# Kernel tuning notes

Hardware: AMD Instinct MI355X
Metric: run time of the kernel (lower is better)

Reference implementation:

```python
import jax, jax.numpy as jnp
import numpy as np

T, B, IN, H, BODY = 512, 256, 128, 512, 64
ALPHA = 10.0 / 100.0  # dt / tau


def setup_inputs() -> dict:
    key = jax.random.key(0)
    ks = jax.random.split(key, 9)
    s = 0.05
    return {
        "x": jax.random.normal(ks[0], (T, B, IN), dtype=jnp.float32),
        "W_i2h": jax.random.normal(ks[1], (H, IN), dtype=jnp.float32) * s,
        "b_i2h": jax.random.normal(ks[2], (H,), dtype=jnp.float32) * s,
        "W_h2h": jax.random.normal(ks[3], (H, H), dtype=jnp.float32) * s,
        "b_h2h": jax.random.normal(ks[4], (H,), dtype=jnp.float32) * s,
        "W_b2h": jax.random.normal(ks[5], (H, BODY), dtype=jnp.float32) * s,
        "b_b2h": jax.random.normal(ks[6], (H,), dtype=jnp.float32) * s,
        "W_h2b": jax.random.normal(ks[7], (BODY, H), dtype=jnp.float32) * s,
        "b_h2b": jax.random.normal(ks[8], (BODY,), dtype=jnp.float32) * s,
        "body_mask": jnp.ones((BODY,), dtype=jnp.float32),
    }


def reference(x, W_i2h, b_i2h, W_h2h, b_h2h, W_b2h, b_b2h, W_h2b, b_h2b, body_mask):
    # Precompute input projection for all timesteps (one big GEMM).
    x_proj = jnp.einsum("tbi,hi->tbh", x, W_i2h) + b_i2h  # [T,B,H]

    def step(carry, xp_t):
        h, b = carry
        pre = xp_t + h @ W_h2h.T + b_h2h + b @ W_b2h.T + b_b2h
        h_new = jax.nn.relu(pre)
        h_new = h * (1.0 - ALPHA) + h_new * ALPHA
        b_new = b * body_mask + ALPHA * (h @ W_h2b.T + b_h2b)
        return (h_new, b_new), (h_new, b_new)

    h0 = jnp.zeros((B, H), dtype=x.dtype)
    b0 = jnp.zeros((B, BODY), dtype=x.dtype)
    (h_fin, _), (hidden_out, body_out) = jax.lax.scan(step, (h0, b0), x_proj)
    return hidden_out, body_out, h_fin
```

## Files before the change

### kernel.cpp

```cpp
#include <hip/hip_runtime.h>


#define T_STEPS 512
#define NB      256
#define IN_DIM  128
#define HID     512
#define BODYD   64
#define ALPHA_F 0.1f

#define WS_WH    0u
#define WS_WH2   524288u
#define WS_WI    1048576u
#define WS_WHB   1179648u
#define WS_WHB2  1245184u
#define WS_WBH   1310720u
#define WS_WBH2  1376256u
#define WS_BIAS  1441792u
#define WS_FLAG  1443840u
#define WS_XCHG  1476608u
#define GRP_STRIDE 73728u

#define BODY_OFF 67108864u
#define FIN_OFF  75497472u

typedef __attribute__((ext_vector_type(8))) short bf16x8;
typedef __attribute__((ext_vector_type(4))) float f32x4;

__device__ __forceinline__ unsigned short f2bf(float f) {
    union { float f; unsigned int u; } v; v.f = f;
    unsigned int u = v.u;
    return (unsigned short)((u + 0x7fffu + ((u >> 16) & 1u)) >> 16);
}
__device__ __forceinline__ float b2f(unsigned short h) {
    union { unsigned int u; float f; } v; v.u = ((unsigned int)h) << 16;
    return v.f;
}
__device__ __forceinline__ bf16x8 ldfrag(const unsigned short* p) {
    return *reinterpret_cast<const bf16x8*>(p);
}

#define LD128_SYSP(dst, ptr)                                           \
    asm volatile("global_load_dwordx4 %0, %1, off sc0 sc1"             \
                 : "=v"(dst) : "v"(ptr) : "memory")
#define ST16_SYS(base, imm, val)                                           \
    asm volatile("global_store_short %0, %1, off offset:" #imm " sc0 sc1"  \
                 :: "v"(base), "v"((unsigned int)(val)) : "memory")

__global__ void init_kernel(const float* __restrict__ Wi2h, const float* __restrict__ bi2h,
                            const float* __restrict__ Whh,  const float* __restrict__ bh2h,
                            const float* __restrict__ Wb2h, const float* __restrict__ bb2h,
                            const float* __restrict__ Wh2b,
                            unsigned char* __restrict__ ws) {
    int idx = blockIdx.x * blockDim.x + threadIdx.x;
    int stride = gridDim.x * blockDim.x;
    unsigned short* WH  = (unsigned short*)(ws + WS_WH);
    unsigned short* WH2 = (unsigned short*)(ws + WS_WH2);
    for (int i = idx; i < HID * HID; i += stride) {
        float w = Whh[i]; unsigned short h = f2bf(w);
        WH[i] = h; WH2[i] = f2bf(w - b2f(h));
    }
    unsigned short* WI = (unsigned short*)(ws + WS_WI);
    for (int i = idx; i < HID * IN_DIM; i += stride) WI[i] = f2bf(Wi2h[i]);
    unsigned short* WHB  = (unsigned short*)(ws + WS_WHB);
    unsigned short* WHB2 = (unsigned short*)(ws + WS_WHB2);
    for (int i = idx; i < BODYD * HID; i += stride) {
        float w = Wh2b[i]; unsigned short h = f2bf(w);
        WHB[i] = h; WHB2[i] = f2bf(w - b2f(h));
    }
    unsigned short* WBH  = (unsigned short*)(ws + WS_WBH);
    unsigned short* WBH2 = (unsigned short*)(ws + WS_WBH2);
    for (int i = idx; i < HID * BODYD; i += stride) {
        float w = Wb2h[i]; unsigned short h = f2bf(w);
        WBH[i] = h; WBH2[i] = f2bf(w - b2f(h));
    }
    float* BS = (float*)(ws + WS_BIAS);
    for (int i = idx; i < HID; i += stride) BS[i] = bi2h[i] + bh2h[i] + bb2h[i];
    unsigned int* Z = (unsigned int*)(ws + WS_FLAG);
    int zn = (int)((WS_XCHG + 32u * GRP_STRIDE - WS_FLAG) / 4u);
    for (int i = idx; i < zn; i += stride) Z[i] = 0u;
}

__global__ __launch_bounds__(256) void xproj_kernel(const float* __restrict__ x,
                                                    float* __restrict__ out,
                                                    const unsigned char* __restrict__ ws) {
    const unsigned short* WI = (const unsigned short*)(ws + WS_WI);
    const float* BS = (const float*)(ws + WS_BIAS);
    int tid = threadIdx.x;
    int l = tid & 63, ww = tid >> 6;
    int lr = l & 15, lq = l >> 4;
    int m0 = blockIdx.x * 64 + ww * 16;
    int n0 = blockIdx.y * 128;

    bf16x8 a[4];
    const float* xr = x + (size_t)(m0 + lr) * IN_DIM + lq * 8;
#pragma unroll
    for (int kt = 0; kt < 4; ++kt) {
        bf16x8 t;
#pragma unroll
        for (int e = 0; e < 8; ++e) t[e] = (short)f2bf(xr[kt * 32 + e]);
        a[kt] = t;
    }
    f32x4 acc[8];
#pragma unroll
    for (int jt = 0; jt < 8; ++jt) acc[jt] = (f32x4){0.f, 0.f, 0.f, 0.f};
#pragma unroll
    for (int jt = 0; jt < 8; ++jt) {
        const unsigned short* wr = WI + (size_t)(n0 + jt * 16 + lr) * IN_DIM + lq * 8;
#pragma unroll
        for (int kt = 0; kt < 4; ++kt) {
            bf16x8 b = ldfrag(wr + kt * 32);
            acc[jt] = __builtin_amdgcn_mfma_f32_16x16x32_bf16(a[kt], b, acc[jt], 0, 0, 0);
        }
    }
#pragma unroll
    for (int jt = 0; jt < 8; ++jt) {
        int n = n0 + jt * 16 + lr;
        float bs = BS[n];
#pragma unroll
        for (int i = 0; i < 4; ++i) {
            int mm = m0 + lq * 4 + i;
            out[(size_t)mm * HID + n] = acc[jt][i] + bs;
        }
    }
}

__global__ __launch_bounds__(512, 2) void rnn_kernel(float* __restrict__ out,
                                                     unsigned char* __restrict__ ws,
                                                     const float* __restrict__ bh2b,
                                                     const float* __restrict__ mask) {
    const int tid = threadIdx.x;
    const int l = tid & 63;
    const int ww = tid >> 6;
    const int jt = ww >> 1;
    const int kh = ww & 1;
    const int lr = l & 15;
    const int lq = l >> 4;

    const int w = blockIdx.x;
    const int xcd = w & 7;
    const int slot = w >> 3;
    const int g = (slot >> 3) * 8 + xcd;
    const int m = slot & 7;

    __shared__ f32x4 stg[1152];
    __shared__ f32x4 lds_h[4][64];
    __shared__ f32x4 lds_b[8][64];
    unsigned char* stgb = (unsigned char*)stg;

    const unsigned short* WH  = (const unsigned short*)(ws + WS_WH);
    const unsigned short* WH2 = (const unsigned short*)(ws + WS_WH2);
    bf16x8 wh[8], wh2[8];
    const int wrow = m * 64 + jt * 16 + lr;
    {
        const unsigned short* p1 = WH  + (size_t)wrow * HID + kh * 256 + lq * 8;
        const unsigned short* p2 = WH2 + (size_t)wrow * HID + kh * 256 + lq * 8;
#pragma unroll
        for (int r = 0; r < 8; ++r) { wh[r] = ldfrag(p1 + r * 32); wh2[r] = ldfrag(p2 + r * 32); }
    }
    const unsigned short* WBH  = (const unsigned short*)(ws + WS_WBH);
    const unsigned short* WBH2 = (const unsigned short*)(ws + WS_WBH2);
    bf16x8 wbh  = ldfrag(WBH  + (size_t)wrow * BODYD + kh * 32 + lq * 8);
    bf16x8 wbh2 = ldfrag(WBH2 + (size_t)wrow * BODYD + kh * 32 + lq * 8);

    bf16x8 whb0 = {}, whb1 = {}, whb0l = {}, whb1l = {};
    float maskv = 0.f, bhbv = 0.f;
    const int kt0 = kh * 8 + 2 * jt;
    if (m < 4) {
        const unsigned short* WHB  = (const unsigned short*)(ws + WS_WHB);
        const unsigned short* WHB2 = (const unsigned short*)(ws + WS_WHB2);
        const int brow = m * 16 + lr;
        whb0  = ldfrag(WHB  + (size_t)brow * HID + kt0 * 32 + lq * 8);
        whb1  = ldfrag(WHB  + (size_t)brow * HID + (kt0 + 1) * 32 + lq * 8);
        whb0l = ldfrag(WHB2 + (size_t)brow * HID + kt0 * 32 + lq * 8);
        whb1l = ldfrag(WHB2 + (size_t)brow * HID + (kt0 + 1) * 32 + lq * 8);
        maskv = mask[m * 16 + lr];
        bhbv  = bh2b[m * 16 + lr];
    }

    unsigned char* xg = ws + WS_XCHG + (size_t)g * GRP_STRIDE;
    unsigned int* flg_self = (unsigned int*)(ws + WS_FLAG) + g * 256 + m * 32;
    unsigned int* flg_base = (unsigned int*)(ws + WS_FLAG) + g * 256;
    unsigned int* flg_mine = flg_base + ww * 32;

    float hst[4] = {0.f, 0.f, 0.f, 0.f};
    float bst[4] = {0.f, 0.f, 0.f, 0.f};

    const int jg = m * 64 + jt * 16 + lr;

    const int c8 = l >> 3;
    const int r8 = l & 7;
    const unsigned char* ghb = xg + (size_t)r8 * 1024 + ww * 128 + c8 * 16;
    unsigned char* sth = stgb + (ww * 8 + c8) * 128 + r8 * 16;
    const int cc = (l >> 3) & 1;
    const unsigned char* gbb = xg + 65536u + (size_t)r8 * 128 + ww * 32 + cc * 16;
    unsigned char* stb = stgb + 16384 + (ww * 2 + cc) * 128 + r8 * 16;
    const bool bl = (ww < 4) && (l < 16);

    const unsigned char* fhb = stgb + kh * 4096 + lq * 128 + (lr & 7) * 16;
    const unsigned char* fbb = stgb + 16384 + (kh * 4 + lq) * 128 + (lr & 7) * 16;

    for (int t = 0; t < T_STEPS; ++t) {
        const int p = t & 1;

        if (t > 0) {
            while (__hip_atomic_load(flg_mine, __ATOMIC_RELAXED,
                                     __HIP_MEMORY_SCOPE_SYSTEM) < (unsigned int)t) {
                __builtin_amdgcn_s_sleep(1);
            }
        }

        const unsigned char* ghp = ghb + (size_t)p * 32768u;
        f32x4 vh1, vh2, vb1, vb2;
        LD128_SYSP(vh1, ghp);
        LD128_SYSP(vh2, ghp + 16384);
        if (bl) {
            const unsigned char* gbp = gbb + (size_t)p * 4096u;
            LD128_SYSP(vb1, gbp);
            LD128_SYSP(vb2, gbp + 2048);
        }
        asm volatile("s_waitcnt vmcnt(0)" ::: "memory");
        __builtin_amdgcn_sched_barrier(0);
        *(f32x4*)sth = vh1;
        *(f32x4*)(sth + 8192) = vh2;
        if (bl) { *(f32x4*)stb = vb1; *(f32x4*)(stb + 1024) = vb2; }
        __syncthreads();

        bf16x8 a[8], a2[8], ab1, ab2;
#pragma unroll
        for (int r = 0; r < 8; ++r) {
            a[r]  = *(const bf16x8*)(fhb + r * 512);
            a2[r] = *(const bf16x8*)(fhb + 8192 + r * 512);
        }
        ab1 = *(const bf16x8*)fbb;
        ab2 = *(const bf16x8*)(fbb + 1024);

        float cpre[4] = {0.f, 0.f, 0.f, 0.f};
        float* op = out + (size_t)t * (NB * HID) + (size_t)(g * 8) * HID + jg;
        if (!kh && lq < 2) {
#pragma unroll
            for (int i = 0; i < 4; ++i)
                cpre[i] = __builtin_nontemporal_load(op + (size_t)(lq * 4 + i) * HID);
        }

        f32x4 acc0 = {0.f, 0.f, 0.f, 0.f}, acc1 = acc0, acc2 = acc0;
#pragma unroll
        for (int r = 0; r < 8; ++r) acc0 = __builtin_amdgcn_mfma_f32_16x16x32_bf16(a[r],  wh[r],  acc0, 0, 0, 0);
#pragma unroll
        for (int r = 0; r < 8; ++r) acc1 = __builtin_amdgcn_mfma_f32_16x16x32_bf16(a2[r], wh[r],  acc1, 0, 0, 0);
#pragma unroll
        for (int r = 0; r < 8; ++r) acc2 = __builtin_amdgcn_mfma_f32_16x16x32_bf16(a[r],  wh2[r], acc2, 0, 0, 0);
        acc0 = __builtin_amdgcn_mfma_f32_16x16x32_bf16(ab1, wbh,  acc0, 0, 0, 0);
        acc1 = __builtin_amdgcn_mfma_f32_16x16x32_bf16(ab2, wbh,  acc1, 0, 0, 0);
        acc2 = __builtin_amdgcn_mfma_f32_16x16x32_bf16(ab1, wbh2, acc2, 0, 0, 0);
        f32x4 acc = acc0 + acc1 + acc2;

        f32x4 bacc = {0.f, 0.f, 0.f, 0.f};
        if (m < 4) {
            bf16x8 s0, s1, u0, u1;
            if      (jt == 0) { s0 = a[0]; s1 = a[1]; u0 = a2[0]; u1 = a2[1]; }
            else if (jt == 1) { s0 = a[2]; s1 = a[3]; u0 = a2[2]; u1 = a2[3]; }
            else if (jt == 2) { s0 = a[4]; s1 = a[5]; u0 = a2[4]; u1 = a2[5]; }
            else              { s0 = a[6]; s1 = a[7]; u0 = a2[6]; u1 = a2[7]; }
            f32x4 b0 = {0.f, 0.f, 0.f, 0.f}, b1 = b0;
            b0 = __builtin_amdgcn_mfma_f32_16x16x32_bf16(s0, whb0,  b0, 0, 0, 0);
            b1 = __builtin_amdgcn_mfma_f32_16x16x32_bf16(s1, whb1,  b1, 0, 0, 0);
            b0 = __builtin_amdgcn_mfma_f32_16x16x32_bf16(u0, whb0,  b0, 0, 0, 0);
            b1 = __builtin_amdgcn_mfma_f32_16x16x32_bf16(u1, whb1,  b1, 0, 0, 0);
            b0 = __builtin_amdgcn_mfma_f32_16x16x32_bf16(s0, whb0l, b0, 0, 0, 0);
            b1 = __builtin_amdgcn_mfma_f32_16x16x32_bf16(s1, whb1l, b1, 0, 0, 0);
            bacc = b0 + b1;
        }

        if (kh) lds_h[jt][l] = acc;
        if (m < 4) lds_b[ww][l] = bacc;
        __syncthreads();

        float hnv[4] = {0.f, 0.f, 0.f, 0.f};
        float bnv[4] = {0.f, 0.f, 0.f, 0.f};

        if (!kh) {
            f32x4 oth = lds_h[jt][l];
            f32x4 sum = acc + oth;
            if (lq < 2) {
                unsigned short* q1 = (unsigned short*)(xg + ((p ^ 1) * 2 + 0) * 16384)
                                     + (lq * 4) * HID + jg;
                unsigned short* q2 = (unsigned short*)(xg + ((p ^ 1) * 2 + 1) * 16384)
                                     + (lq * 4) * HID + jg;
                unsigned short hh[4], hl[4];
#pragma unroll
                for (int i = 0; i < 4; ++i) {
                    float pre = sum[i] + cpre[i];
                    float rl = fmaxf(pre, 0.f);
                    float hv = 0.9f * hst[i] + 0.1f * rl;
                    hst[i] = hv; hnv[i] = hv;
                    hh[i] = f2bf(hv); hl[i] = f2bf(hv - b2f(hh[i]));
                }
                ST16_SYS(q1, 0,    hh[0]); ST16_SYS(q1, 1024, hh[1]);
                ST16_SYS(q1, 2048, hh[2]); ST16_SYS(q1, 3072, hh[3]);
                ST16_SYS(q2, 0,    hl[0]); ST16_SYS(q2, 1024, hl[1]);
                ST16_SYS(q2, 2048, hl[2]); ST16_SYS(q2, 3072, hl[3]);
            }
        }
        if (ww == 0 && m < 4) {
            f32x4 bs = lds_b[0][l];
#pragma unroll
            for (int s = 1; s < 8; ++s) bs += lds_b[s][l];
            if (lq < 2) {
                int jb = m * 16 + lr;
                unsigned short* r1 = (unsigned short*)(xg + 65536 + ((p ^ 1) * 2 + 0) * 2048)
                                     + (lq * 4) * BODYD + jb;
                unsigned short* r2 = (unsigned short*)(xg + 65536 + ((p ^ 1) * 2 + 1) * 2048)
                                     + (lq * 4) * BODYD + jb;
                unsigned short bh[4], blo[4];
#pragma unroll
                for (int i = 0; i < 4; ++i) {
                    float bn = bst[i] * maskv + ALPHA_F * (bs[i] + bhbv);
                    bst[i] = bn; bnv[i] = bn;
                    bh[i] = f2bf(bn); blo[i] = f2bf(bn - b2f(bh[i]));
                }
                ST16_SYS(r1, 0,   bh[0]);  ST16_SYS(r1, 128, bh[1]);
                ST16_SYS(r1, 256, bh[2]);  ST16_SYS(r1, 384, bh[3]);
                ST16_SYS(r2, 0,   blo[0]); ST16_SYS(r2, 128, blo[1]);
                ST16_SYS(r2, 256, blo[2]); ST16_SYS(r2, 384, blo[3]);
            }
        }

        asm volatile("s_waitcnt vmcnt(0)" ::: "memory");
        __syncthreads();

        if (tid == 0) {
            __hip_atomic_store(flg_self, (unsigned int)(t + 1),
                               __ATOMIC_RELAXED, __HIP_MEMORY_SCOPE_SYSTEM);
        }

        if (!kh && lq < 2) {
#pragma unroll
            for (int i = 0; i < 4; ++i)
                __builtin_nontemporal_store(hnv[i], op + (size_t)(lq * 4 + i) * HID);
        }
        if (ww == 0 && m < 4 && lq < 2) {
            int jb = m * 16 + lr;
#pragma unroll
            for (int i = 0; i < 4; ++i) {
                int mi = lq * 4 + i;
                __builtin_nontemporal_store(
                    bnv[i],
                    out + BODY_OFF + (size_t)t * (NB * BODYD) + (size_t)(g * 8 + mi) * BODYD + jb);
            }
        }
    }

    if (!kh && lq < 2) {
#pragma unroll
        for (int i = 0; i < 4; ++i) {
            int mi = lq * 4 + i;
            __builtin_nontemporal_store(hst[i], out + FIN_OFF + (size_t)(g * 8 + mi) * HID + jg);
        }
    }
}

extern "C" void kernel_launch(void* const* d_in, const int* in_sizes, int n_in,
                              void* d_out, int out_size, void* d_ws, size_t ws_size,
                              hipStream_t stream) {
    const float* x    = (const float*)d_in[0];
    const float* Wi2h = (const float*)d_in[1];
    const float* bi2h = (const float*)d_in[2];
    const float* Whh  = (const float*)d_in[3];
    const float* bh2h = (const float*)d_in[4];
    const float* Wb2h = (const float*)d_in[5];
    const float* bb2h = (const float*)d_in[6];
    const float* Wh2b = (const float*)d_in[7];
    const float* bh2b = (const float*)d_in[8];
    const float* mask = (const float*)d_in[9];
    float* out = (float*)d_out;
    unsigned char* ws = (unsigned char*)d_ws;

    init_kernel<<<256, 256, 0, stream>>>(Wi2h, bi2h, Whh, bh2h, Wb2h, bb2h, Wh2b, ws);
    xproj_kernel<<<dim3(2048, 4), 256, 0, stream>>>(x, out, ws);

    void* kargs[] = { (void*)&out, (void*)&ws, (void*)&bh2b, (void*)&mask };
    hipLaunchCooperativeKernel((void*)rnn_kernel, dim3(256), dim3(512), kargs, 0, stream);
}
```

Baseline: 1.777 ms.

## Replace per-block flag with per-wave flags to drop end-of-step block barrier

Each wave that produces hidden or body state now publishes its own completion flag right after its stores drain, instead of waiting on a block-wide __syncthreads and a single flag from thread 0. Consumers poll several per-wave flags in parallel lanes (lanes 0-4) rather than one block flag. Body reduction moves from wave 0 to wave 1 to spread work. This removes a block barrier from the per-timestep critical path, at the cost of more flag traffic and more polling loads per step.

```diff
diff --git a/kernel.cpp b/kernel.cpp
--- a/kernel.cpp
+++ b/kernel.cpp
@@ -180,7 +180,6 @@
     unsigned char* xg = ws + WS_XCHG + (size_t)g * GRP_STRIDE;
     unsigned int* flg_self = (unsigned int*)(ws + WS_FLAG) + g * 256 + m * 32;
     unsigned int* flg_base = (unsigned int*)(ws + WS_FLAG) + g * 256;
-    unsigned int* flg_mine = flg_base + ww * 32;
 
     float hst[4] = {0.f, 0.f, 0.f, 0.f};
     float bst[4] = {0.f, 0.f, 0.f, 0.f};
@@ -191,9 +190,8 @@
     const int r8 = l & 7;
     const unsigned char* ghb = xg + (size_t)r8 * 1024 + ww * 128 + c8 * 16;
     unsigned char* sth = stgb + (ww * 8 + c8) * 128 + r8 * 16;
-    const int cc = (l >> 3) & 1;
-    const unsigned char* gbb = xg + 65536u + (size_t)r8 * 128 + ww * 32 + cc * 16;
-    unsigned char* stb = stgb + 16384 + (ww * 2 + cc) * 128 + r8 * 16;
+    const unsigned char* gbb = xg + 65536u + (size_t)r8 * 128 + ww * 32 + ((l >> 3) & 1) * 16;
+    unsigned char* stb = stgb + 16384 + (ww * 2 + ((l >> 3) & 1)) * 128 + r8 * 16;
     const bool bl = (ww < 4) && (l < 16);
 
     const unsigned char* fhb = stgb + kh * 4096 + lq * 128 + (lr & 7) * 16;
@@ -203,9 +201,13 @@
         const int p = t & 1;
 
         if (t > 0) {
-            while (__hip_atomic_load(flg_mine, __ATOMIC_RELAXED,
-                                     __HIP_MEMORY_SCOPE_SYSTEM) < (unsigned int)t) {
-                __builtin_amdgcn_s_sleep(1);
+            const bool need = (l < 4) || ((l == 4) && (ww < 4));
+            if (need) {
+                unsigned int* f = flg_base + ww * 32 + l;
+                while (__hip_atomic_load(f, __ATOMIC_RELAXED,
+                                         __HIP_MEMORY_SCOPE_SYSTEM) < (unsigned int)t) {
+                    __builtin_amdgcn_s_sleep(1);
+                }
             }
         }
 
@@ -275,12 +277,10 @@
         if (m < 4) lds_b[ww][l] = bacc;
         __syncthreads();
 
-        float hnv[4] = {0.f, 0.f, 0.f, 0.f};
-        float bnv[4] = {0.f, 0.f, 0.f, 0.f};
-
         if (!kh) {
             f32x4 oth = lds_h[jt][l];
             f32x4 sum = acc + oth;
+            float hnv[4] = {0.f, 0.f, 0.f, 0.f};
             if (lq < 2) {
                 unsigned short* q1 = (unsigned short*)(xg + ((p ^ 1) * 2 + 0) * 16384)
                                      + (lq * 4) * HID + jg;
@@ -300,13 +300,25 @@
                 ST16_SYS(q2, 0,    hl[0]); ST16_SYS(q2, 1024, hl[1]);
                 ST16_SYS(q2, 2048, hl[2]); ST16_SYS(q2, 3072, hl[3]);
             }
-        }
-        if (ww == 0 && m < 4) {
+            asm volatile("s_waitcnt vmcnt(0)" ::: "memory");
+            if (l == 0) {
+                __hip_atomic_store(flg_self + jt, (unsigned int)(t + 1),
+                                   __ATOMIC_RELAXED, __HIP_MEMORY_SCOPE_SYSTEM);
+            }
+            if (lq < 2) {
+#pragma unroll
+                for (int i = 0; i < 4; ++i)
+                    __builtin_nontemporal_store(hnv[i], op + (size_t)(lq * 4 + i) * HID);
+            }
+        }
+
+        if (ww == 1 && m < 4) {
             f32x4 bs = lds_b[0][l];
 #pragma unroll
             for (int s = 1; s < 8; ++s) bs += lds_b[s][l];
+            float bnv[4] = {0.f, 0.f, 0.f, 0.f};
+            int jb = m * 16 + lr;
             if (lq < 2) {
-                int jb = m * 16 + lr;
                 unsigned short* r1 = (unsigned short*)(xg + 65536 + ((p ^ 1) * 2 + 0) * 2048)
                                      + (lq * 4) * BODYD + jb;
                 unsigned short* r2 = (unsigned short*)(xg + 65536 + ((p ^ 1) * 2 + 1) * 2048)
@@ -323,29 +335,20 @@
                 ST16_SYS(r2, 0,   blo[0]); ST16_SYS(r2, 128, blo[1]);
                 ST16_SYS(r2, 256, blo[2]); ST16_SYS(r2, 384, blo[3]);
             }
-        }
-
-        asm volatile("s_waitcnt vmcnt(0)" ::: "memory");
-        __syncthreads();
-
-        if (tid == 0) {
-            __hip_atomic_store(flg_self, (unsigned int)(t + 1),
-                               __ATOMIC_RELAXED, __HIP_MEMORY_SCOPE_SYSTEM);
-        }
-
-        if (!kh && lq < 2) {
-#pragma unroll
-            for (int i = 0; i < 4; ++i)
-                __builtin_nontemporal_store(hnv[i], op + (size_t)(lq * 4 + i) * HID);
-        }
-        if (ww == 0 && m < 4 && lq < 2) {
-            int jb = m * 16 + lr;
-#pragma unroll
-            for (int i = 0; i < 4; ++i) {
-                int mi = lq * 4 + i;
-                __builtin_nontemporal_store(
-                    bnv[i],
-                    out + BODY_OFF + (size_t)t * (NB * BODYD) + (size_t)(g * 8 + mi) * BODYD + jb);
+            asm volatile("s_waitcnt vmcnt(0)" ::: "memory");
+            if (l == 0) {
+                __hip_atomic_store(flg_self + 4, (unsigned int)(t + 1),
+                                   __ATOMIC_RELAXED, __HIP_MEMORY_SCOPE_SYSTEM);
+            }
+            if (lq < 2) {
+#pragma unroll
+                for (int i = 0; i < 4; ++i) {
+                    int mi = lq * 4 + i;
+                    __builtin_nontemporal_store(
+                        bnv[i],
+                        out + BODY_OFF + (size_t)t * (NB * BODYD)
+                            + (size_t)(g * 8 + mi) * BODYD + jb);
+                }
             }
         }
     }
```

Result: slower. 2.092 ms (+17.7%).
